# Performance work log

Hardware: AMD Instinct MI355X
Metric: run time of the kernel (lower is better)

Reference implementation:

```python
import jax, jax.numpy as jnp
import numpy as np
import math

HEAD_DIM = 64
RP_DIM = 256
B, H, N = 4, 8, 4096
EPS = 1e-4  # performer positive-feature epsilon


def _ortho_gaussian_matrix(m, d, seed=0):
    # gaussian_orthogonal_random_matrix, scaling=0: stack QR-orthogonalized
    # d x d gaussian blocks, scale rows by norms of an iid gaussian matrix.
    rng = np.random.default_rng(seed)
    blocks = []
    for _ in range(int(np.ceil(m / d))):
        g = rng.standard_normal((d, d))
        q, _ = np.linalg.qr(g)
        blocks.append(q.T)
    mat = np.concatenate(blocks, axis=0)[:m]
    multiplier = np.linalg.norm(rng.standard_normal((m, d)), axis=1)
    return (multiplier[:, None] * mat).astype(np.float32)


def _softmax_features(x, proj, is_query):
    # FAVOR+ positive random features: ratio * exp(Wx - ||x||^2/2 - stab) + eps
    ratio = proj.shape[0] ** -0.5
    xp = jnp.einsum('bhnd,md->bhnm', x, proj)
    diag = 0.5 * jnp.sum(x * x, axis=-1, keepdims=True)
    if is_query:
        stab = jnp.max(xp, axis=-1, keepdims=True)
    else:
        stab = jnp.max(xp, axis=(-1, -2), keepdims=True)
    return ratio * (jnp.exp(xp - diag - stab) + EPS)


def setup_inputs() -> dict:
    key = jax.random.key(0)
    kq, kk, kv = jax.random.split(key, 3)
    Q = jax.random.normal(kq, (B, H, N, HEAD_DIM), dtype=jnp.float32)
    K = jax.random.normal(kk, (B, H, N, HEAD_DIM), dtype=jnp.float32)
    V = jax.random.normal(kv, (B, H, N, HEAD_DIM), dtype=jnp.float32)
    mask = jnp.ones((B, N), dtype=jnp.float32)
    projection = jnp.asarray(_ortho_gaussian_matrix(RP_DIM, HEAD_DIM, seed=0))
    return {'Q': Q, 'K': K, 'V': V, 'mask': mask, 'projection': projection}


def reference(Q, K, V, mask, projection):
    scale = HEAD_DIM ** -0.25  # 1/sqrt(sqrt(head_dim))
    m = mask[:, None, :, None]
    q = Q * scale
    k = K * scale * m
    v = V * m
    phi_q = _softmax_features(q, projection, is_query=True)   # [b,h,n,m]
    phi_k = _softmax_features(k, projection, is_query=False)  # [b,h,n,m]
    # non-causal linear attention
    k_sum = jnp.sum(phi_k, axis=2)                                   # [b,h,m]
    D_inv = 1.0 / jnp.einsum('bhnm,bhm->bhn', phi_q, k_sum)          # [b,h,n]
    context = jnp.einsum('bhnm,bhne->bhme', phi_k, v)                # [b,h,m,e]
    out = jnp.einsum('bhme,bhnm,bhn->bhne', context, phi_q, D_inv)   # [b,h,n,e]
    return out
```

## Files before the change

### kernel.cpp

```cpp
#include <hip/hip_runtime.h>
#include <hip/hip_bf16.h>


typedef __attribute__((ext_vector_type(8))) short short8;
typedef __attribute__((ext_vector_type(4))) float floatx4;

constexpr int BB = 4, HH = 8, NN = 4096, DD = 64, MM = 256, BH = 32;
constexpr int NCH = 16;
constexpr float SCALE = 0.3535533905932738f;
constexpr float RATIO = 0.0625f;
constexpr float EPSI  = 1e-4f;
constexpr float NEGINF = -3.4e38f;

__device__ inline unsigned pk2(float a, float b) {
  unsigned ua = __float_as_uint(a) + 0x8000u;
  unsigned ub = __float_as_uint(b) + 0x8000u;
  return (ua >> 16) | (ub & 0xffff0000u);
}
__device__ inline float hif(float x) {
  return __uint_as_float((__float_as_uint(x) + 0x8000u) & 0xffff0000u);
}
__device__ inline unsigned short bhi(float x) {
  return (unsigned short)((__float_as_uint(x) + 0x8000u) >> 16);
}
__device__ inline int ph16(int i) { return (i & 56) | ((i + (i >> 3)) & 7); }

union Frag { short8 s8; unsigned u[4]; };

__device__ inline void atomicMaxF(float* a, float v) {
  unsigned* ai = (unsigned*)a;
  unsigned old = __atomic_load_n(ai, __ATOMIC_RELAXED);
  while (__uint_as_float(old) < v) {
    unsigned assumed = old;
    old = atomicCAS(ai, assumed, __float_as_uint(v));
    if (old == assumed) break;
  }
}

__global__ __launch_bounds__(256) void prep_kernel(
    const float* __restrict__ proj, unsigned short* __restrict__ projH,
    unsigned short* __restrict__ projL, float* __restrict__ stabk,
    float* __restrict__ Vs, float* __restrict__ ctxsum,
    float* __restrict__ ksE) {
  const int i = blockIdx.x * 256 + threadIdx.x;
  float v = proj[i];
  projH[i] = bhi(v);
  projL[i] = bhi(v - hif(v));
  if (i < BH) stabk[i] = NEGINF;
  if (i < 2048) { Vs[i] = 0.f; ctxsum[i] = 0.f; }
  if (i < 8192) ksE[i] = 0.f;
}

template <bool PARTIAL>
__global__ __launch_bounds__(256) void kside_kernel(
    const float* __restrict__ K, const float* __restrict__ V,
    const float* __restrict__ mask,
    const unsigned short* __restrict__ projH, const unsigned short* __restrict__ projL,
    float* __restrict__ stabk, float* __restrict__ ksE,
    float* __restrict__ ctxOut, float* __restrict__ Vs) {
  const int bh = blockIdx.y, b = bh >> 3;
  const int nch = blockIdx.x & (NCH - 1);
  const int ms  = blockIdx.x >> 4;
  const int t = threadIdx.x;
  const int w = t >> 6, l = t & 63, c = l & 15, sq = l >> 4;
  const int m0 = ms * 128 + w * 32;

  __shared__ __align__(16) unsigned short sK[2][32 * 72];
  __shared__ __align__(16) unsigned short sVt[2][64 * 40];
  __shared__ float sDiag[32];
  __shared__ float sRed[4];
  __shared__ float sVsum[4][64];
  __shared__ __align__(16) unsigned short sPhi[4][2][512];

  Frag Bp[2][2][2];
#pragma unroll
  for (int tt = 0; tt < 2; ++tt)
#pragma unroll
    for (int s = 0; s < 2; ++s) {
      const size_t o = (size_t)(m0 + tt * 16 + c) * DD + s * 32 + sq * 8;
      Bp[tt][s][0].s8 = *(const short8*)&projH[o];
      Bp[tt][s][1].s8 = *(const short8*)&projL[o];
    }

  floatx4 ctxacc[2][4];
#pragma unroll
  for (int i = 0; i < 2; ++i)
#pragma unroll
    for (int j = 0; j < 4; ++j) ctxacc[i][j] = (floatx4){0.f, 0.f, 0.f, 0.f};
  float ksac[2] = {0.f, 0.f};
  float mxloc = NEGINF;
  float vsacc = 0.f;

  const int r0 = nch * 256;

  for (int ch = 0; ch < 8; ++ch) {
    const int rb = r0 + ch * 32;
    __syncthreads();

#pragma unroll
    for (int rep = 0; rep < 2; ++rep) {
      const int f = t + rep * 256;
      const int n = f >> 4, dg = f & 15;
      const float mk = mask[b * NN + rb + n];
      const float msc = mk * SCALE;
      float4 kv = *(const float4*)(K + ((size_t)bh * NN + rb + n) * DD + dg * 4);
      float k0 = kv.x * msc, k1 = kv.y * msc, k2 = kv.z * msc, k3 = kv.w * msc;
      float ss = fmaf(k0, k0, fmaf(k1, k1, fmaf(k2, k2, k3 * k3)));
      ss += __shfl_xor(ss, 1); ss += __shfl_xor(ss, 2);
      ss += __shfl_xor(ss, 4); ss += __shfl_xor(ss, 8);
      if (dg == 0) sDiag[n] = 0.5f * ss;
      unsigned h0 = pk2(k0, k1), h1 = pk2(k2, k3);
      float q0 = k0 - hif(k0), q1 = k1 - hif(k1);
      float q2 = k2 - hif(k2), q3 = k3 - hif(k3);
      *(uint2*)(&sK[0][n * 72 + dg * 4]) = make_uint2(h0, h1);
      *(uint2*)(&sK[1][n * 72 + dg * 4]) = make_uint2(pk2(q0, q1), pk2(q2, q3));
    }

#pragma unroll
    for (int rep = 0; rep < 2; ++rep) {
      const int nb = w * 4 + rep * 16;
      const int n_loc = nb + sq;
      const float mk = mask[b * NN + rb + n_loc];
      float4 vv = *(const float4*)(V + ((size_t)bh * NN + rb + n_loc) * DD + c * 4);
      float va[4] = {vv.x * mk, vv.y * mk, vv.z * mk, vv.w * mk};
      float g[4];
#pragma unroll
      for (int k = 0; k < 4; ++k) {
        const int gi = (sq + k) & 3;
        float sel = va[(sq - k) & 3];
        g[gi] = __shfl(sel, gi * 16 + c);
      }
      const int estar = c * 4 + sq;
      vsacc += ((g[0] + g[1]) + (g[2] + g[3]));
      unsigned h0 = pk2(g[0], g[1]), h1 = pk2(g[2], g[3]);
      float q0 = g[0] - hif(g[0]), q1 = g[1] - hif(g[1]);
      float q2 = g[2] - hif(g[2]), q3 = g[3] - hif(g[3]);
      *(uint2*)(&sVt[0][estar * 40 + nb]) = make_uint2(h0, h1);
      *(uint2*)(&sVt[1][estar * 40 + nb]) = make_uint2(pk2(q0, q1), pk2(q2, q3));
    }
    __syncthreads();

    Frag Ak[2][2][2];
#pragma unroll
    for (int i = 0; i < 2; ++i)
#pragma unroll
      for (int s = 0; s < 2; ++s) {
        Ak[i][s][0].s8 = *(const short8*)&sK[0][(i * 16 + c) * 72 + s * 32 + sq * 8];
        Ak[i][s][1].s8 = *(const short8*)&sK[1][(i * 16 + c) * 72 + s * 32 + sq * 8];
      }
    Frag Bv[4][2];
#pragma unroll
    for (int E = 0; E < 4; ++E) {
      Bv[E][0].s8 = *(const short8*)&sVt[0][(E * 16 + c) * 40 + sq * 8];
      Bv[E][1].s8 = *(const short8*)&sVt[1][(E * 16 + c) * 40 + sq * 8];
    }

#pragma unroll
    for (int tt = 0; tt < 2; ++tt) {
      floatx4 xacc[2];
#pragma unroll
      for (int i = 0; i < 2; ++i) {
        floatx4 a = (floatx4){0.f, 0.f, 0.f, 0.f};
#pragma unroll
        for (int s = 0; s < 2; ++s) {
          a = __builtin_amdgcn_mfma_f32_16x16x32_bf16(Ak[i][s][0].s8, Bp[tt][s][0].s8, a, 0, 0, 0);
          a = __builtin_amdgcn_mfma_f32_16x16x32_bf16(Ak[i][s][0].s8, Bp[tt][s][1].s8, a, 0, 0, 0);
          a = __builtin_amdgcn_mfma_f32_16x16x32_bf16(Ak[i][s][1].s8, Bp[tt][s][0].s8, a, 0, 0, 0);
        }
        xacc[i] = a;
      }
      const int qp_c = sq >> 1, half = (sq & 1) * 4;
#pragma unroll
      for (int i = 0; i < 2; ++i) {
        float p[4];
#pragma unroll
        for (int jj = 0; jj < 4; ++jj) {
          float xp = xacc[i][jj];
          mxloc = fmaxf(mxloc, xp);
          p[jj] = __expf(xp - sDiag[i * 16 + sq * 4 + jj]);
          ksac[tt] += p[jj];
        }
        unsigned h0 = pk2(p[0], p[1]), h1 = pk2(p[2], p[3]);
        float q0 = p[0] - hif(p[0]), q1 = p[1] - hif(p[1]);
        float q2 = p[2] - hif(p[2]), q3 = p[3] - hif(p[3]);
        const int tl = (i * 2 + qp_c) * 16 + c;
        const int idx = ph16(tl) * 8 + half;
        *(uint2*)&sPhi[w][0][idx] = make_uint2(h0, h1);
        *(uint2*)&sPhi[w][1][idx] = make_uint2(pk2(q0, q1), pk2(q2, q3));
      }
      Frag Ap[2];
      Ap[0].s8 = *(const short8*)&sPhi[w][0][ph16(l) * 8];
      Ap[1].s8 = *(const short8*)&sPhi[w][1][ph16(l) * 8];
#pragma unroll
      for (int E = 0; E < 4; ++E) {
        ctxacc[tt][E] = __builtin_amdgcn_mfma_f32_16x16x32_bf16(Ap[0].s8, Bv[E][0].s8, ctxacc[tt][E], 0, 0, 0);
        ctxacc[tt][E] = __builtin_amdgcn_mfma_f32_16x16x32_bf16(Ap[0].s8, Bv[E][1].s8, ctxacc[tt][E], 0, 0, 0);
        ctxacc[tt][E] = __builtin_amdgcn_mfma_f32_16x16x32_bf16(Ap[1].s8, Bv[E][0].s8, ctxacc[tt][E], 0, 0, 0);
      }
    }
  }

#pragma unroll
  for (int tt = 0; tt < 2; ++tt) {
    float v = ksac[tt];
    v += __shfl_xor(v, 16);
    v += __shfl_xor(v, 32);
    if (sq == 0) atomicAdd(&ksE[bh * MM + m0 + tt * 16 + c], v);
  }
#pragma unroll
  for (int off = 1; off <= 32; off <<= 1) mxloc = fmaxf(mxloc, __shfl_xor(mxloc, off));
  if (l == 0) sRed[w] = mxloc;
  sVsum[w][c * 4 + sq] = vsacc;
  __syncthreads();
  if (t == 0)
    atomicMaxF(&stabk[bh], fmaxf(fmaxf(sRed[0], sRed[1]), fmaxf(sRed[2], sRed[3])));
  if (ms == 0 && t < 64)
    atomicAdd(&Vs[bh * DD + t],
              (sVsum[0][t] + sVsum[1][t]) + (sVsum[2][t] + sVsum[3][t]));

  if (PARTIAL) {
    float* cg = ctxOut + ((size_t)(bh * NCH + nch) * MM) * DD;
#pragma unroll
    for (int tt = 0; tt < 2; ++tt)
#pragma unroll
      for (int E = 0; E < 4; ++E)
#pragma unroll
        for (int r = 0; r < 4; ++r)
          cg[(m0 + tt * 16 + sq * 4 + r) * DD + E * 16 + c] = ctxacc[tt][E][r];
  } else {
    float* cg = ctxOut + (size_t)bh * MM * DD;
#pragma unroll
    for (int tt = 0; tt < 2; ++tt)
#pragma unroll
      for (int E = 0; E < 4; ++E)
#pragma unroll
        for (int r = 0; r < 4; ++r)
          atomicAdd(&cg[(m0 + tt * 16 + sq * 4 + r) * DD + E * 16 + c],
                    ctxacc[tt][E][r]);
  }
}

template <int NPARTS>
__global__ __launch_bounds__(256) void fixup_kernel(
    const float* __restrict__ stabk, const float* __restrict__ Vs,
    const float* __restrict__ ksE, const float* __restrict__ ctxParts,
    float* __restrict__ ksum, float* __restrict__ kssum,
    float* __restrict__ ctxsum, unsigned short* __restrict__ ctxTH,
    unsigned short* __restrict__ ctxTL) {
  const int bh = blockIdx.y, mc = blockIdx.x, t = threadIdx.x;
  const float es = __expf(-stabk[bh]);
  const int e = t & 63, g = t >> 6;
  const float vse = EPSI * Vs[bh * DD + e];

  __shared__ float tile[64 * 33];
  __shared__ float cred[256];

  float csum = 0.f;
#pragma unroll
  for (int r = 0; r < 8; ++r) {
    const int ml = r * 4 + g;
    const int m = mc * 32 + ml;
    float x = 0.f;
#pragma unroll
    for (int p = 0; p < NPARTS; ++p)
      x += ctxParts[(((size_t)bh * NPARTS + p) * MM + m) * DD + e];
    float v = RATIO * (es * x + vse);
    csum += v;
    tile[e * 33 + ml] = v;
  }
  cred[t] = csum;
  __syncthreads();
  if (t < 64)
    atomicAdd(&ctxsum[bh * DD + t],
              (cred[t] + cred[t + 64]) + (cred[t + 128] + cred[t + 192]));

  {
    const int ml5 = t & 31, elg = t >> 5;
#pragma unroll
    for (int r = 0; r < 8; ++r) {
      const int el = r * 8 + elg;
      float v = tile[el * 33 + ml5];
      const size_t o = ((size_t)(bh * DD + el)) * MM + mc * 32 + ml5;
      ctxTH[o] = bhi(v);
      ctxTL[o] = bhi(v - hif(v));
    }
  }

  if (mc == 0) {
    __syncthreads();
    const float kv = RATIO * (es * ksE[bh * MM + t] + (float)NN * EPSI);
    ksum[bh * MM + t] = kv;
    cred[t] = kv;
    __syncthreads();
    for (int off = 128; off >= 1; off >>= 1) {
      if (t < off) cred[t] += cred[t + off];
      __syncthreads();
    }
    if (t == 0) kssum[bh] = cred[0];
  }
}

__global__ __launch_bounds__(256, 2) void out_kernel(
    const float* __restrict__ Q,
    const unsigned short* __restrict__ projH, const unsigned short* __restrict__ projL,
    const float* __restrict__ ksum,
    const unsigned short* __restrict__ ctxTH, const unsigned short* __restrict__ ctxTL,
    const float* __restrict__ kssum, const float* __restrict__ ctxsum,
    float* __restrict__ out) {
  const int bh = blockIdx.y;
  const int r0 = blockIdx.x * 64;
  const int t = threadIdx.x, w = t >> 6, l = t & 63, c = l & 15, sq = l >> 4;

  __shared__ __align__(16) unsigned short sQ[2][64 * 80];
  __shared__ __align__(16) unsigned short sP[2][64 * 80];
  __shared__ __align__(16) unsigned short sC[2][64 * 80];
  __shared__ float sKs[256];
  __shared__ float sDiag[64];
  __shared__ __align__(16) unsigned short sPhi[4][2][2][512];

  {
    const int row = t >> 2, q4 = t & 3;
    const float* qp = Q + ((size_t)bh * NN + r0 + row) * DD + q4 * 16;
    float4 t0 = *(const float4*)(qp + 0), t1 = *(const float4*)(qp + 4),
           t2 = *(const float4*)(qp + 8), t3 = *(const float4*)(qp + 12);
    float v[16] = {t0.x, t0.y, t0.z, t0.w, t1.x, t1.y, t1.z, t1.w,
                   t2.x, t2.y, t2.z, t2.w, t3.x, t3.y, t3.z, t3.w};
    float ss = 0.f;
#pragma unroll
    for (int j = 0; j < 16; ++j) { v[j] *= SCALE; ss = fmaf(v[j], v[j], ss); }
    ss += __shfl_xor(ss, 1);
    ss += __shfl_xor(ss, 2);
    if (q4 == 0) sDiag[row] = 0.5f * ss;
    unsigned short* dh = &sQ[0][row * 80 + q4 * 16];
    unsigned short* dl = &sQ[1][row * 80 + q4 * 16];
#pragma unroll
    for (int j = 0; j < 8; ++j) {
      *(unsigned*)&dh[2 * j] = pk2(v[2 * j], v[2 * j + 1]);
      float l0 = v[2 * j] - hif(v[2 * j]), l1 = v[2 * j + 1] - hif(v[2 * j + 1]);
      *(unsigned*)&dl[2 * j] = pk2(l0, l1);
    }
  }
  sKs[t] = ksum[bh * MM + t];
  __syncthreads();

  Frag Bq[2][2];
#pragma unroll
  for (int s = 0; s < 2; ++s)
#pragma unroll
    for (int p = 0; p < 2; ++p)
      Bq[s][p].s8 = *(const short8*)&sQ[p][(w * 16 + c) * 80 + s * 32 + sq * 8];

  const float diagc = sDiag[w * 16 + c];
  floatx4 oacc[4];
#pragma unroll
  for (int E = 0; E < 4; ++E) oacc[E] = (floatx4){0.f, 0.f, 0.f, 0.f};
  float mxacc = NEGINF, dsacc = 0.f;

  for (int mc = 0; mc < 4; ++mc) {
    __syncthreads();
    {
      const int row = t >> 2, q4 = t & 3;
      const size_t gp = (size_t)(mc * 64 + row) * DD + q4 * 16;
      const uint4* ph = (const uint4*)&projH[gp];
      const uint4* pl = (const uint4*)&projL[gp];
      *(uint4*)&sP[0][row * 80 + q4 * 16] = ph[0];
      *(uint4*)&sP[0][row * 80 + q4 * 16 + 8] = ph[1];
      *(uint4*)&sP[1][row * 80 + q4 * 16] = pl[0];
      *(uint4*)&sP[1][row * 80 + q4 * 16 + 8] = pl[1];
      const size_t gc = ((size_t)bh * DD + row) * MM + mc * 64 + q4 * 16;
      const uint4* chh = (const uint4*)&ctxTH[gc];
      const uint4* cll = (const uint4*)&ctxTL[gc];
      *(uint4*)&sC[0][row * 80 + q4 * 16] = chh[0];
      *(uint4*)&sC[0][row * 80 + q4 * 16 + 8] = chh[1];
      *(uint4*)&sC[1][row * 80 + q4 * 16] = cll[0];
      *(uint4*)&sC[1][row * 80 + q4 * 16 + 8] = cll[1];
    }
    __syncthreads();

#pragma unroll
    for (int tt = 0; tt < 4; ++tt) {
      Frag Af[2][2];
#pragma unroll
      for (int s = 0; s < 2; ++s)
#pragma unroll
        for (int p = 0; p < 2; ++p)
          Af[s][p].s8 = *(const short8*)&sP[p][(tt * 16 + c) * 80 + s * 32 + sq * 8];
      floatx4 x = (floatx4){0.f, 0.f, 0.f, 0.f};
#pragma unroll
      for (int s = 0; s < 2; ++s) {
        x = __builtin_amdgcn_mfma_f32_16x16x32_bf16(Af[s][0].s8, Bq[s][0].s8, x, 0, 0, 0);
        x = __builtin_amdgcn_mfma_f32_16x16x32_bf16(Af[s][0].s8, Bq[s][1].s8, x, 0, 0, 0);
        x = __builtin_amdgcn_mfma_f32_16x16x32_bf16(Af[s][1].s8, Bq[s][0].s8, x, 0, 0, 0);
      }
      float p4[4];
#pragma unroll
      for (int jj = 0; jj < 4; ++jj) {
        const float xp = x[jj];
        mxacc = fmaxf(mxacc, xp);
        p4[jj] = __expf(xp - diagc);
        dsacc = fmaf(p4[jj], sKs[mc * 64 + tt * 16 + sq * 4 + jj], dsacc);
      }
      const int kstep = tt >> 1;
      const int tl = ((tt & 1) * 2 + (sq >> 1)) * 16 + c;
      const int off = (sq & 1) * 4;
      float l0 = p4[0] - hif(p4[0]), l1 = p4[1] - hif(p4[1]);
      float l2 = p4[2] - hif(p4[2]), l3 = p4[3] - hif(p4[3]);
      *(uint2*)&sPhi[w][0][kstep][tl * 8 + off] = make_uint2(pk2(p4[0], p4[1]), pk2(p4[2], p4[3]));
      *(uint2*)&sPhi[w][1][kstep][tl * 8 + off] = make_uint2(pk2(l0, l1), pk2(l2, l3));
    }

#pragma unroll
    for (int ks = 0; ks < 2; ++ks) {
      Frag Aph[2];
      Aph[0].s8 = *(const short8*)&sPhi[w][0][ks][l * 8];
      Aph[1].s8 = *(const short8*)&sPhi[w][1][ks][l * 8];
#pragma unroll
      for (int E = 0; E < 4; ++E) {
        Frag Bc0, Bc1;
        Bc0.s8 = *(const short8*)&sC[0][(E * 16 + c) * 80 + ks * 32 + sq * 8];
        Bc1.s8 = *(const short8*)&sC[1][(E * 16 + c) * 80 + ks * 32 + sq * 8];
        oacc[E] = __builtin_amdgcn_mfma_f32_16x16x32_bf16(Aph[0].s8, Bc0.s8, oacc[E], 0, 0, 0);
        oacc[E] = __builtin_amdgcn_mfma_f32_16x16x32_bf16(Aph[0].s8, Bc1.s8, oacc[E], 0, 0, 0);
        oacc[E] = __builtin_amdgcn_mfma_f32_16x16x32_bf16(Aph[1].s8, Bc0.s8, oacc[E], 0, 0, 0);
      }
    }
  }

  mxacc = fmaxf(mxacc, __shfl_xor(mxacc, 16));
  mxacc = fmaxf(mxacc, __shfl_xor(mxacc, 32));
  dsacc += __shfl_xor(dsacc, 16);
  dsacc += __shfl_xor(dsacc, 32);

  const float kss = kssum[bh];
  float fac[4], oinv[4];
#pragma unroll
  for (int jj = 0; jj < 4; ++jj) {
    const int src = sq * 4 + jj;
    const float s_row = __shfl(mxacc, src);
    const float d_row = __shfl(dsacc, src);
    const float f = __expf(s_row) * EPSI;
    fac[jj] = f;
    oinv[jj] = 1.f / (d_row + f * kss);
  }

  const float* csb = ctxsum + bh * DD;
#pragma unroll
  for (int E = 0; E < 4; ++E) {
    const float cse = csb[E * 16 + c];
#pragma unroll
    for (int jj = 0; jj < 4; ++jj) {
      const int row = r0 + w * 16 + sq * 4 + jj;
      out[((size_t)bh * NN + row) * DD + E * 16 + c] =
          (oacc[E][jj] + fac[jj] * cse) * oinv[jj];
    }
  }
}

extern "C" void kernel_launch(void* const* d_in, const int* in_sizes, int n_in,
                              void* d_out, int out_size, void* d_ws, size_t ws_size,
                              hipStream_t stream) {
  const float* Q    = (const float*)d_in[0];
  const float* K    = (const float*)d_in[1];
  const float* V    = (const float*)d_in[2];
  const float* mask = (const float*)d_in[3];
  const float* proj = (const float*)d_in[4];
  float* out = (float*)d_out;

  float* wsf = (float*)d_ws;
  float* stabk  = wsf;
  float* ksum   = wsf + 32;
  float* kssum  = wsf + 8224;
  float* Vs     = wsf + 8256;
  float* ctxsum = wsf + 10304;
  float* ksE    = wsf + 12352;
  unsigned short* projH = (unsigned short*)(wsf + 20544);
  unsigned short* projL = (unsigned short*)(wsf + 28736);
  unsigned short* ctxTH = (unsigned short*)(wsf + 36928);
  unsigned short* ctxTL = (unsigned short*)(wsf + 299072);
  float* ctxBig = wsf + 561216;

  const size_t need_partial = (size_t)(561216 + NCH * BH * MM * DD) * 4;
  const bool partial = ws_size >= need_partial;

  prep_kernel<<<64, 256, 0, stream>>>(proj, projH, projL, stabk, Vs, ctxsum, ksE);

  if (partial) {
    kside_kernel<true><<<dim3(NCH * 2, BH), 256, 0, stream>>>(
        K, V, mask, projH, projL, stabk, ksE, ctxBig, Vs);
    fixup_kernel<NCH><<<dim3(8, BH), 256, 0, stream>>>(
        stabk, Vs, ksE, ctxBig, ksum, kssum, ctxsum, ctxTH, ctxTL);
  } else {
    hipMemsetAsync(ctxBig, 0, (size_t)MM * DD * BH * 4, stream);
    kside_kernel<false><<<dim3(NCH * 2, BH), 256, 0, stream>>>(
        K, V, mask, projH, projL, stabk, ksE, ctxBig, Vs);
    fixup_kernel<1><<<dim3(8, BH), 256, 0, stream>>>(
        stabk, Vs, ksE, ctxBig, ksum, kssum, ctxsum, ctxTH, ctxTL);
  }

  out_kernel<<<dim3(64, BH), 256, 0, stream>>>(
      Q, projH, projL, ksum, ctxTH, ctxTL, kssum, ctxsum, out);
}
```

Before: 256.9 us.

## Load projection and context fragments directly from global memory in out_kernel

The out_kernel no longer stages the projection and context tiles through shared memory each chunk. MFMA fragments are read straight from global (L2/L1-cached) memory, which removes two block barriers per chunk. The Q staging area and the per-wave phi scratch now share one shared-memory buffer, and the min-blocks-per-SM launch bound is dropped. This cuts LDS footprint and synchronisation so more blocks can be resident, at the cost of more global/cache traffic and exposed load latency inside the MFMA loop.

```diff
diff --git a/kernel.cpp b/kernel.cpp
--- a/kernel.cpp
+++ b/kernel.cpp
@@ -300,7 +300,7 @@
   }
 }
 
-__global__ __launch_bounds__(256, 2) void out_kernel(
+__global__ __launch_bounds__(256) void out_kernel(
     const float* __restrict__ Q,
     const unsigned short* __restrict__ projH, const unsigned short* __restrict__ projL,
     const float* __restrict__ ksum,
@@ -311,12 +311,11 @@
   const int r0 = blockIdx.x * 64;
   const int t = threadIdx.x, w = t >> 6, l = t & 63, c = l & 15, sq = l >> 4;
 
-  __shared__ __align__(16) unsigned short sQ[2][64 * 80];
-  __shared__ __align__(16) unsigned short sP[2][64 * 80];
-  __shared__ __align__(16) unsigned short sC[2][64 * 80];
+  __shared__ __align__(16) unsigned short sMem[2 * 64 * 80];
   __shared__ float sKs[256];
   __shared__ float sDiag[64];
-  __shared__ __align__(16) unsigned short sPhi[4][2][2][512];
+#define SQ_(p, idx) sMem[(p) * 5120 + (idx)]
+#define SPHI_(wv, p, ks, idx) sMem[((((wv) * 2 + (p)) * 2 + (ks)) * 512) + (idx)]
 
   {
     const int row = t >> 2, q4 = t & 3;
@@ -331,8 +330,8 @@
     ss += __shfl_xor(ss, 1);
     ss += __shfl_xor(ss, 2);
     if (q4 == 0) sDiag[row] = 0.5f * ss;
-    unsigned short* dh = &sQ[0][row * 80 + q4 * 16];
-    unsigned short* dl = &sQ[1][row * 80 + q4 * 16];
+    unsigned short* dh = &SQ_(0, row * 80 + q4 * 16);
+    unsigned short* dl = &SQ_(1, row * 80 + q4 * 16);
 #pragma unroll
     for (int j = 0; j < 8; ++j) {
       *(unsigned*)&dh[2 * j] = pk2(v[2 * j], v[2 * j + 1]);
@@ -348,43 +347,29 @@
   for (int s = 0; s < 2; ++s)
 #pragma unroll
     for (int p = 0; p < 2; ++p)
-      Bq[s][p].s8 = *(const short8*)&sQ[p][(w * 16 + c) * 80 + s * 32 + sq * 8];
+      Bq[s][p].s8 = *(const short8*)&SQ_(p, (w * 16 + c) * 80 + s * 32 + sq * 8);
 
   const float diagc = sDiag[w * 16 + c];
+  __syncthreads();
+
   floatx4 oacc[4];
 #pragma unroll
   for (int E = 0; E < 4; ++E) oacc[E] = (floatx4){0.f, 0.f, 0.f, 0.f};
   float mxacc = NEGINF, dsacc = 0.f;
 
+  const unsigned short* ctxH_b = ctxTH + (size_t)bh * DD * MM;
+  const unsigned short* ctxL_b = ctxTL + (size_t)bh * DD * MM;
+
   for (int mc = 0; mc < 4; ++mc) {
-    __syncthreads();
-    {
-      const int row = t >> 2, q4 = t & 3;
-      const size_t gp = (size_t)(mc * 64 + row) * DD + q4 * 16;
-      const uint4* ph = (const uint4*)&projH[gp];
-      const uint4* pl = (const uint4*)&projL[gp];
-      *(uint4*)&sP[0][row * 80 + q4 * 16] = ph[0];
-      *(uint4*)&sP[0][row * 80 + q4 * 16 + 8] = ph[1];
-      *(uint4*)&sP[1][row * 80 + q4 * 16] = pl[0];
-      *(uint4*)&sP[1][row * 80 + q4 * 16 + 8] = pl[1];
-      const size_t gc = ((size_t)bh * DD + row) * MM + mc * 64 + q4 * 16;
-      const uint4* chh = (const uint4*)&ctxTH[gc];
-      const uint4* cll = (const uint4*)&ctxTL[gc];
-      *(uint4*)&sC[0][row * 80 + q4 * 16] = chh[0];
-      *(uint4*)&sC[0][row * 80 + q4 * 16 + 8] = chh[1];
-      *(uint4*)&sC[1][row * 80 + q4 * 16] = cll[0];
-      *(uint4*)&sC[1][row * 80 + q4 * 16 + 8] = cll[1];
-    }
-    __syncthreads();
-
 #pragma unroll
     for (int tt = 0; tt < 4; ++tt) {
+      const size_t af = (size_t)(mc * 64 + tt * 16 + c) * DD + sq * 8;
       Frag Af[2][2];
 #pragma unroll
-      for (int s = 0; s < 2; ++s)
-#pragma unroll
-        for (int p = 0; p < 2; ++p)
-          Af[s][p].s8 = *(const short8*)&sP[p][(tt * 16 + c) * 80 + s * 32 + sq * 8];
+      for (int s = 0; s < 2; ++s) {
+        Af[s][0].s8 = *(const short8*)&projH[af + s * 32];
+        Af[s][1].s8 = *(const short8*)&projL[af + s * 32];
+      }
       floatx4 x = (floatx4){0.f, 0.f, 0.f, 0.f};
 #pragma unroll
       for (int s = 0; s < 2; ++s) {
@@ -405,26 +390,29 @@
       const int off = (sq & 1) * 4;
       float l0 = p4[0] - hif(p4[0]), l1 = p4[1] - hif(p4[1]);
       float l2 = p4[2] - hif(p4[2]), l3 = p4[3] - hif(p4[3]);
-      *(uint2*)&sPhi[w][0][kstep][tl * 8 + off] = make_uint2(pk2(p4[0], p4[1]), pk2(p4[2], p4[3]));
-      *(uint2*)&sPhi[w][1][kstep][tl * 8 + off] = make_uint2(pk2(l0, l1), pk2(l2, l3));
+      *(uint2*)&SPHI_(w, 0, kstep, tl * 8 + off) = make_uint2(pk2(p4[0], p4[1]), pk2(p4[2], p4[3]));
+      *(uint2*)&SPHI_(w, 1, kstep, tl * 8 + off) = make_uint2(pk2(l0, l1), pk2(l2, l3));
     }
 
 #pragma unroll
     for (int ks = 0; ks < 2; ++ks) {
       Frag Aph[2];
-      Aph[0].s8 = *(const short8*)&sPhi[w][0][ks][l * 8];
-      Aph[1].s8 = *(const short8*)&sPhi[w][1][ks][l * 8];
+      Aph[0].s8 = *(const short8*)&SPHI_(w, 0, ks, l * 8);
+      Aph[1].s8 = *(const short8*)&SPHI_(w, 1, ks, l * 8);
 #pragma unroll
       for (int E = 0; E < 4; ++E) {
+        const size_t bc = (size_t)(E * 16 + c) * MM + mc * 64 + ks * 32 + sq * 8;
         Frag Bc0, Bc1;
-        Bc0.s8 = *(const short8*)&sC[0][(E * 16 + c) * 80 + ks * 32 + sq * 8];
-        Bc1.s8 = *(const short8*)&sC[1][(E * 16 + c) * 80 + ks * 32 + sq * 8];
+        Bc0.s8 = *(const short8*)&ctxH_b[bc];
+        Bc1.s8 = *(const short8*)&ctxL_b[bc];
         oacc[E] = __builtin_amdgcn_mfma_f32_16x16x32_bf16(Aph[0].s8, Bc0.s8, oacc[E], 0, 0, 0);
         oacc[E] = __builtin_amdgcn_mfma_f32_16x16x32_bf16(Aph[0].s8, Bc1.s8, oacc[E], 0, 0, 0);
         oacc[E] = __builtin_amdgcn_mfma_f32_16x16x32_bf16(Aph[1].s8, Bc0.s8, oacc[E], 0, 0, 0);
       }
     }
   }
+#undef SQ_
+#undef SPHI_
 
   mxacc = fmaxf(mxacc, __shfl_xor(mxacc, 16));
   mxacc = fmaxf(mxacc, __shfl_xor(mxacc, 32));
```

Result: slower. 348.9 us (+35.8%).
